# Optimization experiments

Hardware: AMD Instinct MI355X
Metric: run time of the kernel (lower is better)

Reference implementation:

```python
import jax, jax.numpy as jnp
import numpy as np

E = 8
D_IN = 1024
D_HID = 4096
D_OUT = 1024
N_TOK = 32768  # total tokens; equal split of 4096 per expert


def setup_inputs() -> dict:
    key = jax.random.key(0)
    k_in, k_w1, k_w2 = jax.random.split(key, 3)
    inputs = jax.random.normal(k_in, (N_TOK, D_IN), dtype=jnp.float32)
    expert_size = jnp.full((E,), N_TOK // E, dtype=jnp.int64)
    # reset_parameters: normal(0, 1/sqrt(fan_in)) per expert
    w1 = jax.random.normal(k_w1, (E, D_IN, D_HID), dtype=jnp.float32) / np.sqrt(D_IN)
    b1 = jnp.zeros((E, D_HID), dtype=jnp.float32)
    w2 = jax.random.normal(k_w2, (E, D_HID, D_OUT), dtype=jnp.float32) / np.sqrt(D_HID)
    b2 = jnp.zeros((E, D_OUT), dtype=jnp.float32)
    return {"inputs": inputs, "expert_size": expert_size,
            "w1": w1, "b1": b1, "w2": w2, "b2": b2}


def reference(inputs, expert_size, w1, b1, w2, b2):
    # Grouped GEMM over contiguous per-expert splits. expert_size is equal
    # per expert (N_TOK // E), so the variable-split loop in the torch code
    # collapses to a batched einsum with identical math.
    e = w1.shape[0]
    n, d = inputs.shape
    cap = n // e  # tokens per expert (equal splits)
    x = inputs.reshape(e, cap, d)                       # [E, cap, D_IN]
    h = jnp.einsum('ecd,edh->ech', x, w1) + b1[:, None, :]
    h = jax.nn.gelu(h, approximate=False)               # F.gelu default = erf gelu
    y = jnp.einsum('ech,eho->eco', h, w2) + b2[:, None, :]
    return y.reshape(n, -1)                             # [N_TOK, D_OUT]
```

## Files before the change

kernel.cpp:

```cpp
#include <hip/hip_runtime.h>
#include <hip/hip_bf16.h>
#include <type_traits>

#define NE 8
#define DIN 1024
#define DHID 4096
#define DOUTD 1024
#define NTOK 32768
#define CAP (NTOK / NE)

typedef unsigned short u16;
typedef __attribute__((ext_vector_type(8))) short bf16x8;
typedef __attribute__((ext_vector_type(16))) float f32x16;

template <int I> using ic = std::integral_constant<int, I>;

__device__ __forceinline__ u16 f2bf(float x) {
  unsigned u = __builtin_bit_cast(unsigned, x);
  u += 0x7fffu + ((u >> 16) & 1u);
  return (u16)(u >> 16);
}

__device__ __forceinline__ float gelu_f(float x) {
  float u = 0.7978845608028654f * x * (1.0f + 0.044715f * x * x);
  float t = __expf(-2.0f * fabsf(u));
  float r = __fdividef(2.0f * t, 1.0f + t);
  float th = copysignf(1.0f - r, u);
  return 0.5f * x * (1.0f + th);
}

__device__ __forceinline__ void async_ld16(const void* g, void* l) {
  __builtin_amdgcn_global_load_lds(
      (const __attribute__((address_space(1))) unsigned int*)g,
      (__attribute__((address_space(3))) unsigned int*)l, 16, 0, 0);
}

__global__ __launch_bounds__(256) void convert_bf16_kernel(const float* __restrict__ in,
                                                           u16* __restrict__ out) {
  size_t i = ((size_t)blockIdx.x * 256 + threadIdx.x) * 8;
  float4 a = *(const float4*)(in + i);
  float4 b = *(const float4*)(in + i + 4);
  uint4 o;
  o.x = (unsigned)f2bf(a.x) | ((unsigned)f2bf(a.y) << 16);
  o.y = (unsigned)f2bf(a.z) | ((unsigned)f2bf(a.w) << 16);
  o.z = (unsigned)f2bf(b.x) | ((unsigned)f2bf(b.y) << 16);
  o.w = (unsigned)f2bf(b.z) | ((unsigned)f2bf(b.w) << 16);
  *(uint4*)(out + i) = o;
}

__global__ __launch_bounds__(256) void transpose_bf16_kernel(const float* __restrict__ in,
                                                             u16* __restrict__ out,
                                                             int K, int N) {
  __shared__ __align__(16) u16 tile[64 * 72];
  const int e = blockIdx.z;
  const int n0 = blockIdx.x * 64;
  const int k0 = blockIdx.y * 64;
  const float* inp = in + (size_t)e * K * N;
  u16* outp = out + (size_t)e * N * K;
  const int t = threadIdx.x;
  const int kr = t >> 4;
  const int nc = (t & 15) * 4;
#pragma unroll
  for (int rr = 0; rr < 4; ++rr) {
    int kl = rr * 16 + kr;
    float4 v = *(const float4*)(inp + (size_t)(k0 + kl) * N + n0 + nc);
    tile[(nc + 0) * 72 + kl] = f2bf(v.x);
    tile[(nc + 1) * 72 + kl] = f2bf(v.y);
    tile[(nc + 2) * 72 + kl] = f2bf(v.z);
    tile[(nc + 3) * 72 + kl] = f2bf(v.w);
  }
  __syncthreads();
  const int nr = t >> 3;
  const int kc = (t & 7) * 8;
#pragma unroll
  for (int it = 0; it < 2; ++it) {
    int nl = it * 32 + nr;
    bf16x8 w = *(const bf16x8*)(tile + nl * 72 + kc);
    *(bf16x8*)(outp + (size_t)(n0 + nl) * K + k0 + kc) = w;
  }
}

template <int K, int N, bool GELU_OUT>
__global__ __launch_bounds__(512, 2) void moe_gemm256_kernel(
    const u16* __restrict__ A, const u16* __restrict__ Bt,
    const float* __restrict__ bias, void* __restrict__ Out) {
  extern __shared__ __align__(16) char smem_raw[];
  constexpr int TX = N / 256;
  constexpr int NT = K / 32;
  static_assert(NT % 4 == 0 && NT >= 8, "K-tile count");

  const int bid = blockIdx.x;
  const int e = bid & 7;
  const int idx = bid >> 3;
  const int m0 = (idx / TX) * 256;
  const int n0 = (idx % TX) * 256;

  const u16* Ae = A + (size_t)e * CAP * K;
  const u16* Be = Bt + (size_t)e * N * K;

  const int tid = threadIdx.x;
  const int l = tid & 63;
  const int w = tid >> 6;
  const int wr = w >> 2;
  const int wc = w & 3;
  const int l31 = l & 31;
  const int lhi = l >> 5;

  const char* smL = smem_raw;
  const char* smH = smem_raw + 65536;

  int taoff[4][2], wboff[2][2];
#pragma unroll
  for (int mf = 0; mf < 4; ++mf)
#pragma unroll
    for (int kh = 0; kh < 2; ++kh) {
      int r = wr * 128 + mf * 32 + l31;
      int ku = kh * 2 + lhi;
      int r7 = r & 127;
      int lu = (r >> 7) * 4 + ku;
      taoff[mf][kh] = r7 * 128 + ((lu ^ (r7 & 7)) << 4);
    }
#pragma unroll
  for (int nf = 0; nf < 2; ++nf)
#pragma unroll
    for (int kh = 0; kh < 2; ++kh) {
      int r = wc * 64 + nf * 32 + l31;
      int ku = kh * 2 + lhi;
      int r7 = r & 127;
      int lu = (r >> 7) * 4 + ku;
      wboff[nf][kh] = 16384 + r7 * 128 + ((lu ^ (r7 & 7)) << 4);
    }

  auto mkoff = [&](int sidx, int base0) -> size_t {
    int lrow = sidx >> 3, pu = sidx & 7;
    int lu = pu ^ (lrow & 7);
    int r = lrow + ((lu & 4) << 5);
    return (size_t)(base0 + r) * K + (lu & 3) * 8;
  };
  const u16* gA0 = Ae + mkoff(tid, m0);
  const u16* gA1 = Ae + mkoff(512 + tid, m0);
  const u16* gB0 = Be + mkoff(tid, n0);
  const u16* gB1 = Be + mkoff(512 + tid, n0);
  const int dA0 = tid * 16, dA1 = 8192 + tid * 16;
  const int dB0 = 16384 + tid * 16, dB1 = 24576 + tid * 16;

  f32x16 acc[4][2] = {};

  auto prost = [&](auto SBC, int kb) {
    constexpr int SB = decltype(SBC)::value;
    char* sd = (char*)(((SB >= 2) ? smH : smL) + (SB & 1) * 32768);
    async_ld16((const char*)gA0 + kb, sd + dA0);
    async_ld16((const char*)gA1 + kb, sd + dA1);
    async_ld16((const char*)gB0 + kb, sd + dB0);
    async_ld16((const char*)gB1 + kb, sd + dB1);
  };
  prost(ic<0>{}, 0);
  prost(ic<1>{}, 64);
  prost(ic<2>{}, 128);
  asm volatile("s_waitcnt vmcnt(8)\n\ts_barrier" ::: "memory");

  auto tileb = [&](auto JC, auto STC, auto WNC) {
    constexpr int J = decltype(JC)::value;
    constexpr bool ST = decltype(STC)::value;
    constexpr int WN = decltype(WNC)::value;
    constexpr int SB = (J + 3) & 3;
    constexpr int KOFF = (J + 3) * 64;
    const char* sr = ((J >= 2) ? smH : smL) + (J & 1) * 32768;
    char* sd = (char*)(((SB >= 2) ? smH : smL) + (SB & 1) * 32768);
    bf16x8 wf[2][2], t01[2][2], t23[2][2];
    if constexpr (ST) {
      async_ld16((const char*)gA0 + KOFF, sd + dA0);
      async_ld16((const char*)gA1 + KOFF, sd + dA1);
    }
#pragma unroll
    for (int nf = 0; nf < 2; ++nf)
#pragma unroll
      for (int kh = 0; kh < 2; ++kh) wf[nf][kh] = *(const bf16x8*)(sr + wboff[nf][kh]);
#pragma unroll
    for (int mf = 0; mf < 2; ++mf)
#pragma unroll
      for (int kh = 0; kh < 2; ++kh) t01[mf][kh] = *(const bf16x8*)(sr + taoff[mf][kh]);
    __builtin_amdgcn_s_barrier();
    asm volatile("s_waitcnt lgkmcnt(0)");
    __builtin_amdgcn_s_setprio(1);
#pragma unroll
    for (int kh = 0; kh < 2; ++kh)
#pragma unroll
      for (int mf = 0; mf < 2; ++mf)
#pragma unroll
        for (int nf = 0; nf < 2; ++nf)
          acc[mf][nf] = __builtin_amdgcn_mfma_f32_32x32x16_bf16(
              wf[nf][kh], t01[mf][kh], acc[mf][nf], 0, 0, 0);
    __builtin_amdgcn_s_setprio(0);
    __builtin_amdgcn_s_barrier();
    if constexpr (ST) {
      async_ld16((const char*)gB0 + KOFF, sd + dB0);
      async_ld16((const char*)gB1 + KOFF, sd + dB1);
    }
#pragma unroll
    for (int mf = 0; mf < 2; ++mf)
#pragma unroll
      for (int kh = 0; kh < 2; ++kh) t23[mf][kh] = *(const bf16x8*)(sr + taoff[2 + mf][kh]);
    __builtin_amdgcn_s_barrier();
    asm volatile("s_waitcnt lgkmcnt(0)");
    __builtin_amdgcn_s_setprio(1);
#pragma unroll
    for (int kh = 0; kh < 2; ++kh)
#pragma unroll
      for (int mf = 0; mf < 2; ++mf)
#pragma unroll
        for (int nf = 0; nf < 2; ++nf)
          acc[2 + mf][nf] = __builtin_amdgcn_mfma_f32_32x32x16_bf16(
              wf[nf][kh], t23[mf][kh], acc[2 + mf][nf], 0, 0, 0);
    __builtin_amdgcn_s_setprio(0);
    if constexpr (WN >= 0) {
      asm volatile("s_waitcnt vmcnt(%0)\n\ts_barrier" :: "n"(WN) : "memory");
    }
  };

#pragma unroll 1
  for (int g = 0; g < (NT - 4) / 4; ++g) {
    tileb(ic<0>{}, std::true_type{}, ic<8>{});
    tileb(ic<1>{}, std::true_type{}, ic<8>{});
    tileb(ic<2>{}, std::true_type{}, ic<8>{});
    tileb(ic<3>{}, std::true_type{}, ic<8>{});
    gA0 += 128; gA1 += 128; gB0 += 128; gB1 += 128;
  }
  tileb(ic<0>{}, std::true_type{}, ic<8>{});
  tileb(ic<1>{}, std::false_type{}, ic<4>{});
  tileb(ic<2>{}, std::false_type{}, ic<0>{});
  tileb(ic<3>{}, std::false_type{}, ic<-1>{});

  const float* be = bias + (size_t)e * N;
  const int mrow = m0 + wr * 128 + l31;
  const int ncb = n0 + wc * 64 + lhi * 4;
  if constexpr (GELU_OUT) {
    u16* Oe = (u16*)Out + (size_t)e * (size_t)CAP * N;
#pragma unroll
    for (int mf = 0; mf < 4; ++mf) {
      int m = mrow + mf * 32;
#pragma unroll
      for (int nf = 0; nf < 2; ++nf)
#pragma unroll
        for (int q = 0; q < 4; ++q) {
          int n = ncb + nf * 32 + q * 8;
          float4 bv = *(const float4*)(be + n);
          ushort4 o;
          o.x = f2bf(gelu_f(acc[mf][nf][4 * q + 0] + bv.x));
          o.y = f2bf(gelu_f(acc[mf][nf][4 * q + 1] + bv.y));
          o.z = f2bf(gelu_f(acc[mf][nf][4 * q + 2] + bv.z));
          o.w = f2bf(gelu_f(acc[mf][nf][4 * q + 3] + bv.w));
          *(ushort4*)(Oe + (size_t)m * N + n) = o;
        }
    }
  } else {
    float* Oe = (float*)Out + (size_t)e * (size_t)CAP * N;
#pragma unroll
    for (int mf = 0; mf < 4; ++mf) {
      int m = mrow + mf * 32;
#pragma unroll
      for (int nf = 0; nf < 2; ++nf)
#pragma unroll
        for (int q = 0; q < 4; ++q) {
          int n = ncb + nf * 32 + q * 8;
          float4 bv = *(const float4*)(be + n);
          float4 o;
          o.x = acc[mf][nf][4 * q + 0] + bv.x;
          o.y = acc[mf][nf][4 * q + 1] + bv.y;
          o.z = acc[mf][nf][4 * q + 2] + bv.z;
          o.w = acc[mf][nf][4 * q + 3] + bv.w;
          *(float4*)(Oe + (size_t)m * N + n) = o;
        }
    }
  }
}

extern "C" void kernel_launch(void* const* d_in, const int* in_sizes, int n_in,
                              void* d_out, int out_size, void* d_ws, size_t ws_size,
                              hipStream_t stream) {
  const float* x  = (const float*)d_in[0];
  const float* w1 = (const float*)d_in[2];
  const float* b1 = (const float*)d_in[3];
  const float* w2 = (const float*)d_in[4];
  const float* b2 = (const float*)d_in[5];
  float* out = (float*)d_out;

  char* wsp = (char*)d_ws;
  u16* x_bf = (u16*)(wsp);
  u16* w1t  = (u16*)(wsp + (size_t)67108864);
  u16* w2t  = (u16*)(wsp + (size_t)134217728);
  u16* h    = (u16*)(wsp + (size_t)201326592);

  hipFuncSetAttribute(reinterpret_cast<const void*>(moe_gemm256_kernel<DIN, DHID, true>),
                      hipFuncAttributeMaxDynamicSharedMemorySize, 131072);
  hipFuncSetAttribute(reinterpret_cast<const void*>(moe_gemm256_kernel<DHID, DOUTD, false>),
                      hipFuncAttributeMaxDynamicSharedMemorySize, 131072);

  convert_bf16_kernel<<<(NTOK * DIN) / (256 * 8), 256, 0, stream>>>(x, x_bf);
  transpose_bf16_kernel<<<dim3(DHID / 64, DIN / 64, NE), 256, 0, stream>>>(w1, w1t, DIN, DHID);
  transpose_bf16_kernel<<<dim3(DOUTD / 64, DHID / 64, NE), 256, 0, stream>>>(w2, w2t, DHID, DOUTD);

  moe_gemm256_kernel<DIN, DHID, true>
      <<<dim3(NE * (CAP / 256) * (DHID / 256)), 512, 131072, stream>>>(x_bf, w1t, b1, h);
  moe_gemm256_kernel<DHID, DOUTD, false>
      <<<dim3(NE * (CAP / 256) * (DOUTD / 256)), 512, 131072, stream>>>(h, w2t, b2, out);
}
```

Baseline: 789.8 us.

## Switch GEMM inner loop to 16x16x32 MFMA tiles with split LDS waits

Replaces the 32x32x16 bf16 MFMA fragments with 16x16x32 bf16 MFMAs over an 8x4 grid of 16x16 accumulator tiles per wave, with the LDS offsets and epilogue indexing recomputed to match. All fragment loads for a K-tile are issued up front. The first half of the MFMAs starts after a partial lgkmcnt wait, replacing the two mid-tile barriers with a software wait split. This aims to reduce barrier stalls and overlap LDS reads with compute, at the cost of more MFMA instructions and a different register and bank-access pattern.

```diff
diff --git a/kernel.cpp b/kernel.cpp
--- a/kernel.cpp
+++ b/kernel.cpp
@@ -11,7 +11,7 @@
 
 typedef unsigned short u16;
 typedef __attribute__((ext_vector_type(8))) short bf16x8;
-typedef __attribute__((ext_vector_type(16))) float f32x16;
+typedef __attribute__((ext_vector_type(4))) float f32x4;
 
 template <int I> using ic = std::integral_constant<int, I>;
 
@@ -103,33 +103,27 @@
   const int w = tid >> 6;
   const int wr = w >> 2;
   const int wc = w & 3;
-  const int l31 = l & 31;
-  const int lhi = l >> 5;
+  const int g = l >> 4;
+  const int rl = l & 15;
 
   const char* smL = smem_raw;
   const char* smH = smem_raw + 65536;
 
-  int taoff[4][2], wboff[2][2];
-#pragma unroll
-  for (int mf = 0; mf < 4; ++mf)
-#pragma unroll
-    for (int kh = 0; kh < 2; ++kh) {
-      int r = wr * 128 + mf * 32 + l31;
-      int ku = kh * 2 + lhi;
-      int r7 = r & 127;
-      int lu = (r >> 7) * 4 + ku;
-      taoff[mf][kh] = r7 * 128 + ((lu ^ (r7 & 7)) << 4);
-    }
-#pragma unroll
-  for (int nf = 0; nf < 2; ++nf)
-#pragma unroll
-    for (int kh = 0; kh < 2; ++kh) {
-      int r = wc * 64 + nf * 32 + l31;
-      int ku = kh * 2 + lhi;
-      int r7 = r & 127;
-      int lu = (r >> 7) * 4 + ku;
-      wboff[nf][kh] = 16384 + r7 * 128 + ((lu ^ (r7 & 7)) << 4);
-    }
+  int aoff[8], boff[4];
+#pragma unroll
+  for (int j = 0; j < 8; ++j) {
+    int r = wr * 128 + j * 16 + rl;
+    int r7 = r & 127;
+    int lu = (r >> 7) * 4 + g;
+    aoff[j] = r7 * 128 + ((lu ^ (r7 & 7)) << 4);
+  }
+#pragma unroll
+  for (int i = 0; i < 4; ++i) {
+    int r = wc * 64 + i * 16 + rl;
+    int r7 = r & 127;
+    int lu = (r >> 7) * 4 + g;
+    boff[i] = 16384 + r7 * 128 + ((lu ^ (r7 & 7)) << 4);
+  }
 
   auto mkoff = [&](int sidx, int base0) -> size_t {
     int lrow = sidx >> 3, pu = sidx & 7;
@@ -144,7 +138,7 @@
   const int dA0 = tid * 16, dA1 = 8192 + tid * 16;
   const int dB0 = 16384 + tid * 16, dB1 = 24576 + tid * 16;
 
-  f32x16 acc[4][2] = {};
+  f32x4 acc[8][4] = {};
 
   auto prost = [&](auto SBC, int kb) {
     constexpr int SB = decltype(SBC)::value;
@@ -167,51 +161,32 @@
     constexpr int KOFF = (J + 3) * 64;
     const char* sr = ((J >= 2) ? smH : smL) + (J & 1) * 32768;
     char* sd = (char*)(((SB >= 2) ? smH : smL) + (SB & 1) * 32768);
-    bf16x8 wf[2][2], t01[2][2], t23[2][2];
     if constexpr (ST) {
       async_ld16((const char*)gA0 + KOFF, sd + dA0);
       async_ld16((const char*)gA1 + KOFF, sd + dA1);
-    }
-#pragma unroll
-    for (int nf = 0; nf < 2; ++nf)
-#pragma unroll
-      for (int kh = 0; kh < 2; ++kh) wf[nf][kh] = *(const bf16x8*)(sr + wboff[nf][kh]);
-#pragma unroll
-    for (int mf = 0; mf < 2; ++mf)
-#pragma unroll
-      for (int kh = 0; kh < 2; ++kh) t01[mf][kh] = *(const bf16x8*)(sr + taoff[mf][kh]);
-    __builtin_amdgcn_s_barrier();
-    asm volatile("s_waitcnt lgkmcnt(0)");
-    __builtin_amdgcn_s_setprio(1);
-#pragma unroll
-    for (int kh = 0; kh < 2; ++kh)
-#pragma unroll
-      for (int mf = 0; mf < 2; ++mf)
-#pragma unroll
-        for (int nf = 0; nf < 2; ++nf)
-          acc[mf][nf] = __builtin_amdgcn_mfma_f32_32x32x16_bf16(
-              wf[nf][kh], t01[mf][kh], acc[mf][nf], 0, 0, 0);
-    __builtin_amdgcn_s_setprio(0);
-    __builtin_amdgcn_s_barrier();
-    if constexpr (ST) {
       async_ld16((const char*)gB0 + KOFF, sd + dB0);
       async_ld16((const char*)gB1 + KOFF, sd + dB1);
     }
-#pragma unroll
-    for (int mf = 0; mf < 2; ++mf)
-#pragma unroll
-      for (int kh = 0; kh < 2; ++kh) t23[mf][kh] = *(const bf16x8*)(sr + taoff[2 + mf][kh]);
-    __builtin_amdgcn_s_barrier();
+    bf16x8 bfr[4], afr[8];
+#pragma unroll
+    for (int i = 0; i < 4; ++i) bfr[i] = *(const bf16x8*)(sr + boff[i]);
+#pragma unroll
+    for (int j = 0; j < 8; ++j) afr[j] = *(const bf16x8*)(sr + aoff[j]);
+    asm volatile("s_waitcnt lgkmcnt(4)");
+    __builtin_amdgcn_sched_barrier(0);
+    __builtin_amdgcn_s_setprio(1);
+#pragma unroll
+    for (int j = 0; j < 4; ++j)
+#pragma unroll
+      for (int i = 0; i < 4; ++i)
+        acc[j][i] = __builtin_amdgcn_mfma_f32_16x16x32_bf16(bfr[i], afr[j], acc[j][i], 0, 0, 0);
     asm volatile("s_waitcnt lgkmcnt(0)");
-    __builtin_amdgcn_s_setprio(1);
-#pragma unroll
-    for (int kh = 0; kh < 2; ++kh)
-#pragma unroll
-      for (int mf = 0; mf < 2; ++mf)
-#pragma unroll
-        for (int nf = 0; nf < 2; ++nf)
-          acc[2 + mf][nf] = __builtin_amdgcn_mfma_f32_32x32x16_bf16(
-              wf[nf][kh], t23[mf][kh], acc[2 + mf][nf], 0, 0, 0);
+    __builtin_amdgcn_sched_barrier(0);
+#pragma unroll
+    for (int j = 4; j < 8; ++j)
+#pragma unroll
+      for (int i = 0; i < 4; ++i)
+        acc[j][i] = __builtin_amdgcn_mfma_f32_16x16x32_bf16(bfr[i], afr[j], acc[j][i], 0, 0, 0);
     __builtin_amdgcn_s_setprio(0);
     if constexpr (WN >= 0) {
       asm volatile("s_waitcnt vmcnt(%0)\n\ts_barrier" :: "n"(WN) : "memory");
@@ -219,7 +194,7 @@
   };
 
 #pragma unroll 1
-  for (int g = 0; g < (NT - 4) / 4; ++g) {
+  for (int gq = 0; gq < (NT - 4) / 4; ++gq) {
     tileb(ic<0>{}, std::true_type{}, ic<8>{});
     tileb(ic<1>{}, std::true_type{}, ic<8>{});
     tileb(ic<2>{}, std::true_type{}, ic<8>{});
@@ -232,45 +207,41 @@
   tileb(ic<3>{}, std::false_type{}, ic<-1>{});
 
   const float* be = bias + (size_t)e * N;
-  const int mrow = m0 + wr * 128 + l31;
-  const int ncb = n0 + wc * 64 + lhi * 4;
+  const int mb = m0 + wr * 128 + rl;
+  const int nb = n0 + wc * 64 + g * 4;
   if constexpr (GELU_OUT) {
     u16* Oe = (u16*)Out + (size_t)e * (size_t)CAP * N;
 #pragma unroll
-    for (int mf = 0; mf < 4; ++mf) {
-      int m = mrow + mf * 32;
-#pragma unroll
-      for (int nf = 0; nf < 2; ++nf)
-#pragma unroll
-        for (int q = 0; q < 4; ++q) {
-          int n = ncb + nf * 32 + q * 8;
-          float4 bv = *(const float4*)(be + n);
-          ushort4 o;
-          o.x = f2bf(gelu_f(acc[mf][nf][4 * q + 0] + bv.x));
-          o.y = f2bf(gelu_f(acc[mf][nf][4 * q + 1] + bv.y));
-          o.z = f2bf(gelu_f(acc[mf][nf][4 * q + 2] + bv.z));
-          o.w = f2bf(gelu_f(acc[mf][nf][4 * q + 3] + bv.w));
-          *(ushort4*)(Oe + (size_t)m * N + n) = o;
-        }
+    for (int j = 0; j < 8; ++j) {
+      int m = mb + j * 16;
+#pragma unroll
+      for (int i = 0; i < 4; ++i) {
+        int n = nb + i * 16;
+        float4 bv = *(const float4*)(be + n);
+        ushort4 o;
+        o.x = f2bf(gelu_f(acc[j][i][0] + bv.x));
+        o.y = f2bf(gelu_f(acc[j][i][1] + bv.y));
+        o.z = f2bf(gelu_f(acc[j][i][2] + bv.z));
+        o.w = f2bf(gelu_f(acc[j][i][3] + bv.w));
+        *(ushort4*)(Oe + (size_t)m * N + n) = o;
+      }
     }
   } else {
     float* Oe = (float*)Out + (size_t)e * (size_t)CAP * N;
 #pragma unroll
-    for (int mf = 0; mf < 4; ++mf) {
-      int m = mrow + mf * 32;
-#pragma unroll
-      for (int nf = 0; nf < 2; ++nf)
-#pragma unroll
-        for (int q = 0; q < 4; ++q) {
-          int n = ncb + nf * 32 + q * 8;
-          float4 bv = *(const float4*)(be + n);
-          float4 o;
-          o.x = acc[mf][nf][4 * q + 0] + bv.x;
-          o.y = acc[mf][nf][4 * q + 1] + bv.y;
-          o.z = acc[mf][nf][4 * q + 2] + bv.z;
-          o.w = acc[mf][nf][4 * q + 3] + bv.w;
-          *(float4*)(Oe + (size_t)m * N + n) = o;
-        }
+    for (int j = 0; j < 8; ++j) {
+      int m = mb + j * 16;
+#pragma unroll
+      for (int i = 0; i < 4; ++i) {
+        int n = nb + i * 16;
+        float4 bv = *(const float4*)(be + n);
+        float4 o;
+        o.x = acc[j][i][0] + bv.x;
+        o.y = acc[j][i][1] + bv.y;
+        o.z = acc[j][i][2] + bv.z;
+        o.w = acc[j][i][3] + bv.w;
+        *(float4*)(Oe + (size_t)m * N + n) = o;
+      }
     }
   }
 }
```

Result: faster. 739.1 us (-6.4%).
